# Kernel tuning notes

Hardware: AMD Instinct MI355X
Metric: run time of the kernel (lower is better)

## Reference

```python
import jax, jax.numpy as jnp
import numpy as np

VOCAB, P, K, B, L, R = 50257, 512, 64, 32, 2048, 5


def setup_inputs() -> dict:
    key = jax.random.key(0)
    k1, k2, k3, k4, k5, k6, k7 = jax.random.split(key, 7)
    return {
        "x": jax.random.randint(k1, (B, L), 0, VOCAB, dtype=jnp.int32),
        "V": jax.random.normal(k2, (VOCAB, P), dtype=jnp.float32),
        "C": jax.random.normal(k3, (K, P), dtype=jnp.float32),
        "f1_w": jax.random.normal(k4, (2 * R + 1,), dtype=jnp.float32),
        "f1_b": jax.random.normal(k5, (K,), dtype=jnp.float32),
        "f2_w": jax.random.normal(k6, (K, P), dtype=jnp.float32),
        "f2_b": jax.random.normal(k7, (K,), dtype=jnp.float32),
    }


def reference(x, V, C, f1_w, f1_b, f2_w, f2_b):
    b, l = x.shape
    k, p = C.shape
    w = f1_w.shape[0]
    r = (w - 1) // 2
    emb = V[x]                                              # [B,L,P] embedding lookup
    x_hat = emb / jnp.linalg.norm(emb, axis=2, keepdims=True)
    l_hat = C / jnp.linalg.norm(C, axis=1, keepdims=True)
    G = jnp.einsum('kp,blp->bkl', l_hat, x_hat)             # cosine sim [B,K,L]
    # sliding-window dot product == depthwise 1D cross-correlation, 'same' padding
    u = jax.lax.conv_general_dilated(
        G.reshape(b * k, 1, l), f1_w.reshape(1, 1, w),
        window_strides=(1,), padding=[(r, r)],
        dimension_numbers=('NCH', 'OIH', 'NCH'),
    ).reshape(b, k, l)
    m = jax.nn.relu(u + f1_b[None, :, None])                # [B,K,L]
    beta = jax.nn.softmax(m.max(axis=1), axis=1)            # max over labels, softmax over seq -> [B,L]
    pooled = jnp.mean(beta[:, :, None] * emb, axis=1)       # [B,P]
    return pooled @ f2_w.T + f2_b                           # [B,K]
```

## Files before the change

kernel.cpp:

```cpp
#include <hip/hip_runtime.h>
#include <hip/hip_bf16.h>

#define PP     512
#define KK     64
#define BB     32
#define LLEN   2048
#define SROWS  74

typedef __attribute__((ext_vector_type(8)))  short short8;
typedef __attribute__((ext_vector_type(16))) float float16;

__device__ inline unsigned int pack_bf2(float lo, float hi) {
    __hip_bfloat162 h = __float22bfloat162_rn(make_float2(lo, hi));
    unsigned int u;
    __builtin_memcpy(&u, &h, 4);
    return u;
}
__device__ inline float bf_lo(unsigned int v) { return __uint_as_float(v << 16); }
__device__ inline float bf_hi(unsigned int v) { return __uint_as_float(v & 0xffff0000u); }

__global__ void k1_prep(const float* __restrict__ C, const float* __restrict__ f2w,
                        ushort* __restrict__ Bu) {
    const int n = blockIdx.x;
    const float* src = (n < 64) ? (C + n * PP) : (f2w + (n - 64) * PP);
    const int t = threadIdx.x;
    float v0 = src[t];
    float v1 = src[t + 256];
    __shared__ float red[256];
    red[t] = v0 * v0 + v1 * v1;
    __syncthreads();
    for (int s = 128; s > 0; s >>= 1) {
        if (t < s) red[t] += red[t + s];
        __syncthreads();
    }
    const float inv = (n < 64) ? rsqrtf(red[0]) : 1.f;
    Bu[(((t >> 3)       * 128 + n) << 3) + (t & 7)] = (ushort)(pack_bf2(v0 * inv, 0.f) & 0xffffu);
    Bu[((((t + 256) >> 3)) * 128 + n) * 8 + (t & 7)] = (ushort)(pack_bf2(v1 * inv, 0.f) & 0xffffu);
}

__launch_bounds__(512, 4)
__global__ void k2_fused(const int* __restrict__ x, const float* __restrict__ V,
                         const uint4* __restrict__ Bu4,
                         const float* __restrict__ f1w, const float* __restrict__ f1b,
                         float* __restrict__ pool) {
    __shared__ uint4 sA[SROWS * 64];
    __shared__ int   stok[SROWS];
    __shared__ float rnorm[SROWS];
    __shared__ float smv[64];
    __shared__ float sp[64];
    __shared__ float sscal[2];

    const int tid  = threadIdx.x;
    const int lane = tid & 63;
    const int wv   = tid >> 6;
    const int l31  = lane & 31;
    const int b    = blockIdx.x >> 5;
    const int l0   = (blockIdx.x & 31) * 64;

    if (tid < SROWS) {
        int gl = l0 - 5 + tid;
        gl = min(max(gl, 0), LLEN - 1);
        stok[tid] = x[b * LLEN + tid < SROWS ? gl : 0];
    }
    __syncthreads();

    {
        const int o = tid & 7;
        const int r = tid >> 3;
        const float* src = V + (size_t)stok[r] * PP + o * 4;
        const int swzr = r & 7;
        float nrm = 0.f;
        float4 pa[8];
#pragma unroll
        for (int g = 0; g < 8; ++g) pa[g] = ((const float4*)src)[g * 8];
        float4 pb[8];
#pragma unroll
        for (int g = 0; g < 8; ++g) pb[g] = ((const float4*)src)[(g + 8) * 8];
#pragma unroll
        for (int g = 0; g < 8; ++g) {
            const float4 a = pa[g];
            nrm = fmaf(a.x, a.x, fmaf(a.y, a.y, fmaf(a.z, a.z, fmaf(a.w, a.w, nrm))));
            uint2 w2; w2.x = pack_bf2(a.x, a.y); w2.y = pack_bf2(a.z, a.w);
            const int f = g * 4 + (o >> 1);
            ((uint2*)&sA[r * 64 + (f ^ swzr)])[o & 1] = w2;
        }
#pragma unroll
        for (int g = 0; g < 8; ++g) {
            const float4 a = pb[g];
            nrm = fmaf(a.x, a.x, fmaf(a.y, a.y, fmaf(a.z, a.z, fmaf(a.w, a.w, nrm))));
            uint2 w2; w2.x = pack_bf2(a.x, a.y); w2.y = pack_bf2(a.z, a.w);
            const int f = (g + 8) * 4 + (o >> 1);
            ((uint2*)&sA[r * 64 + (f ^ swzr)])[o & 1] = w2;
        }
        nrm += __shfl_xor(nrm, 1, 64);
        nrm += __shfl_xor(nrm, 2, 64);
        nrm += __shfl_xor(nrm, 4, 64);
        if (o == 0) rnorm[r] = rsqrtf(nrm);
    }
    if (tid < 160) {
        const int h16 = tid & 15;
        const int r   = 64 + (tid >> 4);
        const float* src = V + (size_t)stok[r] * PP + h16 * 4;
        const int swzr = r & 7;
        float nrm = 0.f;
        float4 ph[8];
#pragma unroll
        for (int g = 0; g < 8; ++g) ph[g] = ((const float4*)src)[g * 16];
#pragma unroll
        for (int g = 0; g < 8; ++g) {
            const float4 a = ph[g];
            nrm = fmaf(a.x, a.x, fmaf(a.y, a.y, fmaf(a.z, a.z, fmaf(a.w, a.w, nrm))));
            uint2 w2; w2.x = pack_bf2(a.x, a.y); w2.y = pack_bf2(a.z, a.w);
            const int f = g * 8 + (h16 >> 1);
            ((uint2*)&sA[r * 64 + (f ^ swzr)])[h16 & 1] = w2;
        }
        nrm += __shfl_xor(nrm, 1, 64);
        nrm += __shfl_xor(nrm, 2, 64);
        nrm += __shfl_xor(nrm, 4, 64);
        nrm += __shfl_xor(nrm, 8, 64);
        if (h16 == 0) rnorm[r] = rsqrtf(nrm);
    }
    __syncthreads();

    float16 c0, c1;
#pragma unroll
    for (int i = 0; i < 16; ++i) { c0[i] = 0.f; c1[i] = 0.f; }

    if (wv < 5) {
        const int rowBase = (wv == 0) ? 0 : (wv == 1) ? 32 : (wv == 2) ? 42
                          : (wv == 3) ? 5 : 37;
        const int nh    = (wv < 3) ? 0 : 64;
        const int cc    = lane >> 5;
        const int row   = rowBase + l31;
        const int abase = row * 64;
        const int aswz  = row & 7;
#pragma unroll 8
        for (int ks = 0; ks < 32; ++ks) {
            const int ff = ks * 2 + cc;
            const uint4 av = sA[abase + (ff ^ aswz)];
            const uint4 b0 = Bu4[ff * 128 + nh + l31];
            const uint4 b1 = Bu4[ff * 128 + nh + 32 + l31];
            short8 a8, t0, t1;
            __builtin_memcpy(&a8, &av, 16);
            __builtin_memcpy(&t0, &b0, 16);
            __builtin_memcpy(&t1, &b1, 16);
            c0 = __builtin_amdgcn_mfma_f32_32x32x16_bf16(a8, t0, c0, 0, 0, 0);
            c1 = __builtin_amdgcn_mfma_f32_32x32x16_bf16(a8, t1, c1, 0, 0, 0);
        }
    }
    __syncthreads();

    unsigned int* G32 = (unsigned int*)sA;
    float*        E2s = (float*)((char*)sA + 10240);
    float*        sred = (float*)((char*)sA + 28672);
    const int cc = lane >> 5;
    if (wv < 3) {
        const int rowBase = (wv == 0) ? 0 : (wv == 1) ? 32 : 42;
#pragma unroll
        for (int reg = 0; reg < 16; ++reg) {
            const int rr  = (reg & 3) + 8 * (reg >> 2) + 4 * cc;
            const int row = rowBase + rr;
            if (wv == 2 && row < 64) continue;
            const int gl = l0 - 5 + row;
            unsigned int vpk = 0u;
            if (gl >= 0 && gl < LLEN) {
                const float rn = rnorm[row];
                vpk = pack_bf2(c0[reg] * rn, c1[reg] * rn);
            }
            G32[row * 32 + l31] = vpk;
        }
    } else if (wv < 5) {
        const int rowBase = (wv == 3) ? 5 : 37;
#pragma unroll
        for (int reg = 0; reg < 16; ++reg) {
            const int rr = (reg & 3) + 8 * (reg >> 2) + 4 * cc;
            const int o  = rowBase - 5 + rr;
            E2s[o * 64 + l31]      = c0[reg];
            E2s[o * 64 + 32 + l31] = c1[reg];
        }
    }
    __syncthreads();

    float w[11];
#pragma unroll
    for (int t = 0; t < 11; ++t) w[t] = f1w[t];
    const int j = l31;
    const int h = tid >> 5;
    const float bias0 = f1b[j], bias1 = f1b[j + 32];
#pragma unroll
    for (int i = 0; i < 4; ++i) {
        const int o = i * 16 + h;
        float u0 = 0.f, u1 = 0.f;
#pragma unroll
        for (int tap = 0; tap < 11; ++tap) {
            const unsigned int v = G32[(o + tap) * 32 + j];
            u0 = fmaf(bf_lo(v), w[tap], u0);
            u1 = fmaf(bf_hi(v), w[tap], u1);
        }
        float m = fmaxf(fmaxf(u0 + bias0, 0.f), fmaxf(u1 + bias1, 0.f));
#pragma unroll
        for (int off = 16; off > 0; off >>= 1)
            m = fmaxf(m, __shfl_xor(m, off, 64));
        if (j == 0) smv[o] = m;
    }
    __syncthreads();

    if (tid < 64) {
        float v = smv[tid];
#pragma unroll
        for (int off = 32; off > 0; off >>= 1)
            v = fmaxf(v, __shfl_xor(v, off, 64));
        if (tid == 0) sscal[0] = v;
    }
    __syncthreads();
    const float mx = sscal[0];
    if (tid < 64) sp[tid] = __expf(smv[tid] - mx);
    __syncthreads();
    if (tid < 64) {
        float s = sp[tid];
#pragma unroll
        for (int off = 32; off > 0; off >>= 1)
            s += __shfl_xor(s, off, 64);
        if (tid == 0) sscal[1] = s;
    }

    float a0 = 0.f, a1 = 0.f;
#pragma unroll
    for (int i = 0; i < 4; ++i) {
        const int o = i * 16 + h;
        const float wgt = sp[o];
        a0 = fmaf(wgt, E2s[o * 64 + j], a0);
        a1 = fmaf(wgt, E2s[o * 64 + 32 + j], a1);
    }
    __syncthreads();
    sred[h * 64 + j]      = a0;
    sred[h * 64 + j + 32] = a1;
    __syncthreads();
    if (tid < 64) {
        float r = 0.f;
#pragma unroll
        for (int hh = 0; hh < 16; ++hh) r += sred[hh * 64 + tid];
        float* dst = pool + (size_t)blockIdx.x * 68;
        dst[tid] = r;
        if (tid == 0) { dst[64] = sscal[0]; dst[65] = sscal[1]; }
    }
}

__global__ void k6_final(const float* __restrict__ pool, const float* __restrict__ f2b,
                         float* __restrict__ out) {
    const int b = blockIdx.x;
    const int k = threadIdx.x;
    float M = -1e30f;
#pragma unroll
    for (int c = 0; c < 32; ++c)
        M = fmaxf(M, pool[(size_t)(b * 32 + c) * 68 + 64]);
    float tot = 0.f, num = 0.f;
#pragma unroll
    for (int c = 0; c < 32; ++c) {
        const float* pc = pool + (size_t)(b * 32 + c) * 68;
        const float sc = __expf(pc[64] - M);
        tot = fmaf(sc, pc[65], tot);
        num = fmaf(sc, pc[k], num);
    }
    out[b * KK + k] = (num / tot) * (1.f / 2048.f) + f2b[k];
}

extern "C" void kernel_launch(void* const* d_in, const int* in_sizes, int n_in,
                              void* d_out, int out_size, void* d_ws, size_t ws_size,
                              hipStream_t stream) {
    const int*   x   = (const int*)d_in[0];
    const float* V   = (const float*)d_in[1];
    const float* C   = (const float*)d_in[2];
    const float* f1w = (const float*)d_in[3];
    const float* f1b = (const float*)d_in[4];
    const float* f2w = (const float*)d_in[5];
    const float* f2b = (const float*)d_in[6];
    float* out = (float*)d_out;

    float* ws = (float*)d_ws;
    ushort* Bu = (ushort*)ws;
    float* pool = ws + 32768;

    k1_prep <<<128, 256, 0, stream>>>(C, f2w, Bu);
    k2_fused<<<BB * 32, 512, 0, stream>>>(x, V, (const uint4*)Bu, f1w, f1b, pool);
    k6_final<<<BB, 64, 0, stream>>>(pool, f2b, out);
}
```

Baseline: 170.0 us.

## Split embedding staging into two K-halves to halve LDS and raise occupancy

The fused kernel now stages the gathered embedding rows into shared memory in two halves of the feature dimension, running the MFMA accumulation after each half. This halves the shared A tile so more blocks fit per CU, and launch bounds are raised from 4 to 6 blocks to match. The cost is an extra pair of barriers and a serialised load-then-compute phase per half, with tighter register limits that could cause spills. The token index load expression is also fixed to index with the clamped position directly.

Measured after the change: 228.1 us. 34.1% more time.

```diff
diff --git a/kernel.cpp b/kernel.cpp
--- a/kernel.cpp
+++ b/kernel.cpp
@@ -38,12 +38,12 @@
     Bu[((((t + 256) >> 3)) * 128 + n) * 8 + (t & 7)] = (ushort)(pack_bf2(v1 * inv, 0.f) & 0xffffu);
 }
 
-__launch_bounds__(512, 4)
+__launch_bounds__(512, 6)
 __global__ void k2_fused(const int* __restrict__ x, const float* __restrict__ V,
                          const uint4* __restrict__ Bu4,
                          const float* __restrict__ f1w, const float* __restrict__ f1b,
                          float* __restrict__ pool) {
-    __shared__ uint4 sA[SROWS * 64];
+    __shared__ uint4 sA[SROWS * 32];
     __shared__ int   stok[SROWS];
     __shared__ float rnorm[SROWS];
     __shared__ float smv[64];
@@ -60,102 +60,96 @@
     if (tid < SROWS) {
         int gl = l0 - 5 + tid;
         gl = min(max(gl, 0), LLEN - 1);
-        stok[tid] = x[b * LLEN + tid < SROWS ? gl : 0];
-    }
-    __syncthreads();
-
-    {
-        const int o = tid & 7;
-        const int r = tid >> 3;
-        const float* src = V + (size_t)stok[r] * PP + o * 4;
-        const int swzr = r & 7;
-        float nrm = 0.f;
-        float4 pa[8];
-#pragma unroll
-        for (int g = 0; g < 8; ++g) pa[g] = ((const float4*)src)[g * 8];
-        float4 pb[8];
-#pragma unroll
-        for (int g = 0; g < 8; ++g) pb[g] = ((const float4*)src)[(g + 8) * 8];
-#pragma unroll
-        for (int g = 0; g < 8; ++g) {
-            const float4 a = pa[g];
-            nrm = fmaf(a.x, a.x, fmaf(a.y, a.y, fmaf(a.z, a.z, fmaf(a.w, a.w, nrm))));
-            uint2 w2; w2.x = pack_bf2(a.x, a.y); w2.y = pack_bf2(a.z, a.w);
-            const int f = g * 4 + (o >> 1);
-            ((uint2*)&sA[r * 64 + (f ^ swzr)])[o & 1] = w2;
-        }
-#pragma unroll
-        for (int g = 0; g < 8; ++g) {
-            const float4 a = pb[g];
-            nrm = fmaf(a.x, a.x, fmaf(a.y, a.y, fmaf(a.z, a.z, fmaf(a.w, a.w, nrm))));
-            uint2 w2; w2.x = pack_bf2(a.x, a.y); w2.y = pack_bf2(a.z, a.w);
-            const int f = (g + 8) * 4 + (o >> 1);
-            ((uint2*)&sA[r * 64 + (f ^ swzr)])[o & 1] = w2;
-        }
-        nrm += __shfl_xor(nrm, 1, 64);
-        nrm += __shfl_xor(nrm, 2, 64);
-        nrm += __shfl_xor(nrm, 4, 64);
-        if (o == 0) rnorm[r] = rsqrtf(nrm);
-    }
-    if (tid < 160) {
-        const int h16 = tid & 15;
-        const int r   = 64 + (tid >> 4);
-        const float* src = V + (size_t)stok[r] * PP + h16 * 4;
-        const int swzr = r & 7;
-        float nrm = 0.f;
-        float4 ph[8];
-#pragma unroll
-        for (int g = 0; g < 8; ++g) ph[g] = ((const float4*)src)[g * 16];
-#pragma unroll
-        for (int g = 0; g < 8; ++g) {
-            const float4 a = ph[g];
-            nrm = fmaf(a.x, a.x, fmaf(a.y, a.y, fmaf(a.z, a.z, fmaf(a.w, a.w, nrm))));
-            uint2 w2; w2.x = pack_bf2(a.x, a.y); w2.y = pack_bf2(a.z, a.w);
-            const int f = g * 8 + (h16 >> 1);
-            ((uint2*)&sA[r * 64 + (f ^ swzr)])[h16 & 1] = w2;
-        }
-        nrm += __shfl_xor(nrm, 1, 64);
-        nrm += __shfl_xor(nrm, 2, 64);
-        nrm += __shfl_xor(nrm, 4, 64);
-        nrm += __shfl_xor(nrm, 8, 64);
-        if (h16 == 0) rnorm[r] = rsqrtf(nrm);
-    }
-    __syncthreads();
+        stok[tid] = x[b * LLEN + gl];
+    }
+    __syncthreads();
+
+    const int o  = tid & 7;
+    const int r  = tid >> 3;
+    const int rh = 64 + (tid >> 3);
+    float nrmM = 0.f, nrmH = 0.f;
 
     float16 c0, c1;
 #pragma unroll
     for (int i = 0; i < 16; ++i) { c0[i] = 0.f; c1[i] = 0.f; }
 
-    if (wv < 5) {
-        const int rowBase = (wv == 0) ? 0 : (wv == 1) ? 32 : (wv == 2) ? 42
-                          : (wv == 3) ? 5 : 37;
-        const int nh    = (wv < 3) ? 0 : 64;
-        const int cc    = lane >> 5;
-        const int row   = rowBase + l31;
-        const int abase = row * 64;
-        const int aswz  = row & 7;
+    const int rowBase = (wv == 0) ? 0 : (wv == 1) ? 32 : (wv == 2) ? 42
+                      : (wv == 3) ? 5 : 37;
+    const int nh    = (wv < 3) ? 0 : 64;
+    const int cc    = lane >> 5;
+    const int arow  = rowBase + l31;
+    const int abase = arow * 32;
+    const int aswz  = arow & 7;
+
+#pragma unroll
+    for (int p = 0; p < 2; ++p) {
+        {
+            const float4* srcF4 = (const float4*)(V + (size_t)stok[r] * PP) + p * 64 + o;
+            float4 pv[8];
+#pragma unroll
+            for (int g = 0; g < 8; ++g) pv[g] = srcF4[g * 8];
+#pragma unroll
+            for (int g = 0; g < 8; ++g) {
+                const float4 a = pv[g];
+                nrmM = fmaf(a.x, a.x, fmaf(a.y, a.y, fmaf(a.z, a.z, fmaf(a.w, a.w, nrmM))));
+                uint2 w2; w2.x = pack_bf2(a.x, a.y); w2.y = pack_bf2(a.z, a.w);
+                const int fi = g * 8 + o;
+                ((uint2*)&sA[r * 32 + ((fi >> 1) ^ (r & 7))])[fi & 1] = w2;
+            }
+        }
+        if (tid < 80) {
+            const float4* srcF4 = (const float4*)(V + (size_t)stok[rh] * PP) + p * 64 + o;
+            float4 pv[8];
+#pragma unroll
+            for (int g = 0; g < 8; ++g) pv[g] = srcF4[g * 8];
+#pragma unroll
+            for (int g = 0; g < 8; ++g) {
+                const float4 a = pv[g];
+                nrmH = fmaf(a.x, a.x, fmaf(a.y, a.y, fmaf(a.z, a.z, fmaf(a.w, a.w, nrmH))));
+                uint2 w2; w2.x = pack_bf2(a.x, a.y); w2.y = pack_bf2(a.z, a.w);
+                const int fi = g * 8 + o;
+                ((uint2*)&sA[rh * 32 + ((fi >> 1) ^ (rh & 7))])[fi & 1] = w2;
+            }
+        }
+        if (p == 1) {
+            float nm = nrmM;
+            nm += __shfl_xor(nm, 1, 64);
+            nm += __shfl_xor(nm, 2, 64);
+            nm += __shfl_xor(nm, 4, 64);
+            if (o == 0) rnorm[r] = rsqrtf(nm);
+            if (tid < 80) {
+                float nh2 = nrmH;
+                nh2 += __shfl_xor(nh2, 1, 64);
+                nh2 += __shfl_xor(nh2, 2, 64);
+                nh2 += __shfl_xor(nh2, 4, 64);
+                if (o == 0) rnorm[rh] = rsqrtf(nh2);
+            }
+        }
+        __syncthreads();
+
+        if (wv < 5) {
 #pragma unroll 8
-        for (int ks = 0; ks < 32; ++ks) {
-            const int ff = ks * 2 + cc;
-            const uint4 av = sA[abase + (ff ^ aswz)];
-            const uint4 b0 = Bu4[ff * 128 + nh + l31];
-            const uint4 b1 = Bu4[ff * 128 + nh + 32 + l31];
-            short8 a8, t0, t1;
-            __builtin_memcpy(&a8, &av, 16);
-            __builtin_memcpy(&t0, &b0, 16);
-            __builtin_memcpy(&t1, &b1, 16);
-            c0 = __builtin_amdgcn_mfma_f32_32x32x16_bf16(a8, t0, c0, 0, 0, 0);
-            c1 = __builtin_amdgcn_mfma_f32_32x32x16_bf16(a8, t1, c1, 0, 0, 0);
-        }
-    }
-    __syncthreads();
+            for (int ks = 0; ks < 16; ++ks) {
+                const int fl = ks * 2 + cc;
+                const int ff = p * 32 + fl;
+                const uint4 av = sA[abase + (fl ^ aswz)];
+                const uint4 b0 = Bu4[ff * 128 + nh + l31];
+                const uint4 b1 = Bu4[ff * 128 + nh + 32 + l31];
+                short8 a8, t0, t1;
+                __builtin_memcpy(&a8, &av, 16);
+                __builtin_memcpy(&t0, &b0, 16);
+                __builtin_memcpy(&t1, &b1, 16);
+                c0 = __builtin_amdgcn_mfma_f32_32x32x16_bf16(a8, t0, c0, 0, 0, 0);
+                c1 = __builtin_amdgcn_mfma_f32_32x32x16_bf16(a8, t1, c1, 0, 0, 0);
+            }
+        }
+        __syncthreads();
+    }
 
     unsigned int* G32 = (unsigned int*)sA;
-    float*        E2s = (float*)((char*)sA + 10240);
-    float*        sred = (float*)((char*)sA + 28672);
-    const int cc = lane >> 5;
+    float*        E2s = (float*)((char*)sA + 9472);
+    float*        sred = (float*)((char*)sA + 25856);
     if (wv < 3) {
-        const int rowBase = (wv == 0) ? 0 : (wv == 1) ? 32 : 42;
 #pragma unroll
         for (int reg = 0; reg < 16; ++reg) {
             const int rr  = (reg & 3) + 8 * (reg >> 2) + 4 * cc;
@@ -170,13 +164,12 @@
             G32[row * 32 + l31] = vpk;
         }
     } else if (wv < 5) {
-        const int rowBase = (wv == 3) ? 5 : 37;
 #pragma unroll
         for (int reg = 0; reg < 16; ++reg) {
             const int rr = (reg & 3) + 8 * (reg >> 2) + 4 * cc;
-            const int o  = rowBase - 5 + rr;
-            E2s[o * 64 + l31]      = c0[reg];
-            E2s[o * 64 + 32 + l31] = c1[reg];
+            const int oo = rowBase - 5 + rr;
+            E2s[oo * 64 + l31]      = c0[reg];
+            E2s[oo * 64 + 32 + l31] = c1[reg];
         }
     }
     __syncthreads();
@@ -189,11 +182,11 @@
     const float bias0 = f1b[j], bias1 = f1b[j + 32];
 #pragma unroll
     for (int i = 0; i < 4; ++i) {
-        const int o = i * 16 + h;
+        const int oo = i * 16 + h;
         float u0 = 0.f, u1 = 0.f;
 #pragma unroll
         for (int tap = 0; tap < 11; ++tap) {
-            const unsigned int v = G32[(o + tap) * 32 + j];
+            const unsigned int v = G32[(oo + tap) * 32 + j];
             u0 = fmaf(bf_lo(v), w[tap], u0);
             u1 = fmaf(bf_hi(v), w[tap], u1);
         }
@@ -201,7 +194,7 @@
 #pragma unroll
         for (int off = 16; off > 0; off >>= 1)
             m = fmaxf(m, __shfl_xor(m, off, 64));
-        if (j == 0) smv[o] = m;
+        if (j == 0) smv[oo] = m;
     }
     __syncthreads();
 
@@ -227,21 +220,21 @@
     float a0 = 0.f, a1 = 0.f;
 #pragma unroll
     for (int i = 0; i < 4; ++i) {
-        const int o = i * 16 + h;
-        const float wgt = sp[o];
-        a0 = fmaf(wgt, E2s[o * 64 + j], a0);
-        a1 = fmaf(wgt, E2s[o * 64 + 32 + j], a1);
+        const int oo = i * 16 + h;
+        const float wgt = sp[oo];
+        a0 = fmaf(wgt, E2s[oo * 64 + j], a0);
+        a1 = fmaf(wgt, E2s[oo * 64 + 32 + j], a1);
     }
     __syncthreads();
     sred[h * 64 + j]      = a0;
     sred[h * 64 + j + 32] = a1;
     __syncthreads();
     if (tid < 64) {
-        float r = 0.f;
-#pragma unroll
-        for (int hh = 0; hh < 16; ++hh) r += sred[hh * 64 + tid];
+        float rr = 0.f;
+#pragma unroll
+        for (int hh = 0; hh < 16; ++hh) rr += sred[hh * 64 + tid];
         float* dst = pool + (size_t)blockIdx.x * 68;
-        dst[tid] = r;
+        dst[tid] = rr;
         if (tid == 0) { dst[64] = sscal[0]; dst[65] = sscal[1]; }
     }
 }
```
